# Performance work log

Hardware: AMD Instinct MI355X
Metric: run time of the kernel (lower is better)

Reference implementation:

```python
import jax, jax.numpy as jnp
import numpy as np


def setup_inputs() -> dict:
    key = jax.random.key(0)
    k1, k2 = jax.random.split(key)
    B, S, D = 32, 1024, 384
    MAX_MEL_LEN = 8192  # >= max possible sum of durations (7*1024)
    x = jax.random.normal(k1, (B, S, D), dtype=jnp.float32)
    duration = jax.random.randint(k2, (B, S), 0, 8, dtype=jnp.int32)
    return {"x": x, "duration": duration, "max_mel_len": MAX_MEL_LEN}


def reference(x, duration, max_mel_len):
    # x: (B, S, D) float, duration: (B, S) int, max_mel_len: python int
    B, S, D = x.shape
    csum = jnp.cumsum(duration, axis=1)          # (B, S) inclusive cumsum
    mel_len = csum[:, -1]                        # (B,) expanded length per sample
    t = jnp.arange(max_mel_len, dtype=csum.dtype)  # (T,) output frame indices
    # frame t maps to token i where csum[i-1] <= t < csum[i]; side='right'
    # correctly skips zero-duration tokens (repeated csum values)
    idx = jax.vmap(lambda c: jnp.searchsorted(c, t, side='right'))(csum)  # (B, T)
    idx = jnp.clip(idx, 0, S - 1)
    out = jnp.take_along_axis(x, idx[:, :, None], axis=1)  # (B, T, D) gather
    mask = t[None, :] < mel_len[:, None]                   # (B, T) pad mask
    out = out * mask[:, :, None].astype(x.dtype)
    return out, mel_len.astype(jnp.int64)
```

## Files before the change

### kernel.cpp

```cpp
#include <hip/hip_runtime.h>


#define BATCH 32
#define SRC_S 1024
#define DIM   384
#define ROWS  64
#define C4    (DIM / 4)
#define NXCD  8

typedef float f32x4 __attribute__((ext_vector_type(4)));
typedef int   i32x4 __attribute__((ext_vector_type(4)));

__device__ int g_csum[BATCH * SRC_S];
__device__ int g_mel[BATCH];

__global__ __launch_bounds__(256)
void lr_csum_kernel(const int* __restrict__ duration, float* __restrict__ mel_out) {
    __shared__ int wsum[4];
    const int b = blockIdx.x;
    const int tid = threadIdx.x;
    const int lane = tid & 63;
    const int wid = tid >> 6;

    const i32x4 d = ((const i32x4*)(duration + b * SRC_S))[tid];
    const int s0 = d.x;
    const int s1 = s0 + d.y;
    const int s2 = s1 + d.z;
    const int s3 = s2 + d.w;
    int tot = s3;
    #pragma unroll
    for (int off = 1; off < 64; off <<= 1) {
        const int n = __shfl_up(tot, off, 64);
        if (lane >= off) tot += n;
    }
    if (lane == 63) wsum[wid] = tot;
    __syncthreads();
    int base = 0;
    #pragma unroll
    for (int w = 0; w < 3; ++w) base += (w < wid) ? wsum[w] : 0;
    const int pre = base + tot - s3;

    i32x4 c;
    c.x = pre + s0; c.y = pre + s1; c.z = pre + s2; c.w = pre + s3;
    ((i32x4*)(g_csum + b * SRC_S))[tid] = c;

    if (tid == 255) {
        const int mel = pre + s3;
        g_mel[b] = mel;
        mel_out[b] = (float)mel;
    }
}

__global__ __launch_bounds__(256)
void lr_gather_kernel(const f32x4* __restrict__ x4, f32x4* __restrict__ out4, int T) {
    const int l = blockIdx.x;
    const int xcd = l & (NXCD - 1);
    const int j = l >> 3;
    const int wpb = 8192 / ROWS;
    const int b = xcd + NXCD * (j >> 7);
    const int t0 = (j & (wpb - 1)) * ROWS;
    const int tid = threadIdx.x;

    f32x4* __restrict__ ob = out4 + ((size_t)b * T + t0) * C4;
    const int mel = g_mel[b];

    if (t0 >= mel) {
        const f32x4 z = (f32x4)(0.f);
        #pragma unroll
        for (int k = 0; k < (ROWS * C4) / 256; ++k)
            ob[tid + k * 256] = z;
        return;
    }

    __shared__ int src[ROWS];
    const int* __restrict__ cb = g_csum + b * SRC_S;
    const i32x4 c = ((const i32x4*)cb)[tid];
    const int prev = (tid == 0) ? 0 : cb[4 * tid - 1];

    if (tid < ROWS) src[tid] = -1;
    __syncthreads();

    const int st[4] = {prev, c.x, c.y, c.z};
    const int en[4] = {c.x, c.y, c.z, c.w};
    #pragma unroll
    for (int e = 0; e < 4; ++e) {
        const int lo = (st[e] > t0) ? st[e] : t0;
        const int hi = (en[e] < t0 + ROWS) ? en[e] : (t0 + ROWS);
        const int off = (tid * 4 + e) * C4;
        for (int t = lo; t < hi; ++t) src[t - t0] = off;
    }
    __syncthreads();

    const f32x4* __restrict__ xb = x4 + (size_t)b * SRC_S * C4;
    #pragma unroll
    for (int k = 0; k < (ROWS * C4) / 256; ++k) {
        const int i = tid + k * 256;
        const int row = i / C4;
        const int col = i - row * C4;
        const int o = src[row];
        f32x4 v = (f32x4)(0.f);
        if (o >= 0) v = xb[o + col];
        ob[i] = v;
    }
}

extern "C" void kernel_launch(void* const* d_in, const int* in_sizes, int n_in,
                              void* d_out, int out_size, void* d_ws, size_t ws_size,
                              hipStream_t stream) {
    const float* x = (const float*)d_in[0];
    const int* duration = (const int*)d_in[1];
    const int T = (out_size - BATCH) / (BATCH * DIM);

    float* out = (float*)d_out;
    float* mel_out = out + (size_t)BATCH * T * DIM;

    lr_csum_kernel<<<BATCH, 256, 0, stream>>>(duration, mel_out);

    const int nblocks = BATCH * (T / ROWS);
    lr_gather_kernel<<<nblocks, 256, 0, stream>>>((const f32x4*)x,
                                                  (f32x4*)out, T);
}
```

Baseline: 449.6 us.

## Replace per-frame gather with per-token scatter plus separate zero-fill blocks

```diff
diff --git a/kernel.cpp b/kernel.cpp
--- a/kernel.cpp
+++ b/kernel.cpp
@@ -4,11 +4,10 @@
 #define BATCH 32
 #define SRC_S 1024
 #define DIM   384
-#define ROWS  64
-#define C4    (DIM / 4)
-#define NXCD  8
+#define C2    (DIM / 2)
+#define ZROWS 64
 
-typedef float f32x4 __attribute__((ext_vector_type(4)));
+typedef float f32x2 __attribute__((ext_vector_type(2)));
 typedef int   i32x4 __attribute__((ext_vector_type(4)));
 
 __device__ int g_csum[BATCH * SRC_S];
@@ -51,57 +50,39 @@
     }
 }
 
-__global__ __launch_bounds__(256)
-void lr_gather_kernel(const f32x4* __restrict__ x4, f32x4* __restrict__ out4, int T) {
+__global__ __launch_bounds__(192)
+void lr_scatter_kernel(const f32x2* __restrict__ x2, f32x2* __restrict__ out2,
+                       int T) {
     const int l = blockIdx.x;
-    const int xcd = l & (NXCD - 1);
-    const int j = l >> 3;
-    const int wpb = 8192 / ROWS;
-    const int b = xcd + NXCD * (j >> 7);
-    const int t0 = (j & (wpb - 1)) * ROWS;
     const int tid = threadIdx.x;
+    const int nzf = BATCH * (T / ZROWS);
 
-    f32x4* __restrict__ ob = out4 + ((size_t)b * T + t0) * C4;
-    const int mel = g_mel[b];
-
-    if (t0 >= mel) {
-        const f32x4 z = (f32x4)(0.f);
-        #pragma unroll
-        for (int k = 0; k < (ROWS * C4) / 256; ++k)
-            ob[tid + k * 256] = z;
+    if (l < nzf) {
+        const int nw = T / ZROWS;
+        const int b = l / nw;
+        const int t0 = (l - b * nw) * ZROWS;
+        const int mel = g_mel[b];
+        const int start = (mel > t0) ? mel : t0;
+        const int end = t0 + ZROWS;
+        if (start >= end) return;
+        const f32x2 zz = {0.f, 0.f};
+        f32x2* __restrict__ o = out2 + ((size_t)b * T + start) * C2 + tid;
+        for (int m = start; m < end; ++m) { *o = zz; o += C2; }
         return;
     }
 
-    __shared__ int src[ROWS];
+    const int r = l - nzf;
+    const int b = r >> 10;
+    const int i = r & (SRC_S - 1);
+
+    const f32x2 v = x2[(size_t)(b * SRC_S + i) * C2 + tid];
+
     const int* __restrict__ cb = g_csum + b * SRC_S;
-    const i32x4 c = ((const i32x4*)cb)[tid];
-    const int prev = (tid == 0) ? 0 : cb[4 * tid - 1];
+    const int prev = (i == 0) ? 0 : cb[i - 1];
+    const int cur = cb[i];
 
-    if (tid < ROWS) src[tid] = -1;
-    __syncthreads();
-
-    const int st[4] = {prev, c.x, c.y, c.z};
-    const int en[4] = {c.x, c.y, c.z, c.w};
-    #pragma unroll
-    for (int e = 0; e < 4; ++e) {
-        const int lo = (st[e] > t0) ? st[e] : t0;
-        const int hi = (en[e] < t0 + ROWS) ? en[e] : (t0 + ROWS);
-        const int off = (tid * 4 + e) * C4;
-        for (int t = lo; t < hi; ++t) src[t - t0] = off;
-    }
-    __syncthreads();
-
-    const f32x4* __restrict__ xb = x4 + (size_t)b * SRC_S * C4;
-    #pragma unroll
-    for (int k = 0; k < (ROWS * C4) / 256; ++k) {
-        const int i = tid + k * 256;
-        const int row = i / C4;
-        const int col = i - row * C4;
-        const int o = src[row];
-        f32x4 v = (f32x4)(0.f);
-        if (o >= 0) v = xb[o + col];
-        ob[i] = v;
-    }
+    f32x2* __restrict__ o = out2 + ((size_t)b * T + prev) * C2 + tid;
+    for (int m = prev; m < cur; ++m) { *o = v; o += C2; }
 }
 
 extern "C" void kernel_launch(void* const* d_in, const int* in_sizes, int n_in,
@@ -116,7 +97,7 @@
 
     lr_csum_kernel<<<BATCH, 256, 0, stream>>>(duration, mel_out);
 
-    const int nblocks = BATCH * (T / ROWS);
-    lr_gather_kernel<<<nblocks, 256, 0, stream>>>((const f32x4*)x,
-                                                  (f32x4*)out, T);
+    const int nblocks = BATCH * (T / ZROWS) + BATCH * SRC_S;
+    lr_scatter_kernel<<<nblocks, 192, 0, stream>>>((const f32x2*)x,
+                                                   (f32x2*)out, T);
 }
```

New measurement: 433.9 us. 3.5% less time.
